# Kernel optimization log

Hardware: AMD Instinct MI355X
Metric: run time of the kernel (lower is better)

Reference implementation:

```python
import jax, jax.numpy as jnp
import numpy as np

B, H, HKV, S, D = 1, 16, 4, 2048, 128


def setup_inputs() -> dict:
    key = jax.random.key(0)
    kq, kk, kv = jax.random.split(key, 3)
    Q = jax.random.normal(kq, (B, H, S, D), dtype=jnp.float32)
    K = jax.random.normal(kk, (B, HKV, S, D), dtype=jnp.float32)
    V = jax.random.normal(kv, (B, HKV, S, D), dtype=jnp.float32)
    return {"Q": Q, "K": K, "V": V, "causal": 1, "gqa_group_size": 4}


def reference(Q, K, V, causal, gqa_group_size):
    b, h, s, d = Q.shape
    scale = 1.0 / (d ** 0.5)
    if gqa_group_size > 1:
        # repeat_interleave along head dim: [B,Hkv,S,D] -> [B,H,S,D]
        K = jnp.repeat(K, gqa_group_size, axis=1)
        V = jnp.repeat(V, gqa_group_size, axis=1)
    # scores: [B,H,S,S]
    P = jnp.einsum('bhqd,bhkd->bhqk', Q, K) * scale
    if causal:
        mask = jnp.tril(jnp.ones((s, s), dtype=bool))
        P = jnp.where(mask, P, -jnp.inf)
    P = jax.nn.softmax(P.astype(jnp.float32), axis=-1).astype(Q.dtype)
    O = jnp.einsum('bhqk,bhkd->bhqd', P, V)
    return O
```

## Files before the change

kernel.cpp:

```cpp
#include <hip/hip_runtime.h>
#include <hip/hip_bf16.h>


#define NH    16
#define NHKV  4
#define SEQ   2048
#define DIM   128
#define QBLK  64
#define KVBLK 64
#define NT    (SEQ / KVBLK)

typedef __attribute__((ext_vector_type(8))) short bf16x8_t;
typedef __attribute__((ext_vector_type(4))) float f32x4_t;

__device__ inline ushort f2bf(float f) {
    uint x = __float_as_uint(f);
    uint r = (x + 0x7fffu + ((x >> 16) & 1u)) >> 16;
    return (ushort)r;
}

#define GLOAD_LDS16(gsrc, ldst) \
    __builtin_amdgcn_global_load_lds( \
        (const __attribute__((address_space(1))) void*)(gsrc), \
        (__attribute__((address_space(3))) void*)(ldst), 16, 0, 0)

extern "C" __global__ __launch_bounds__(256)
void prep_kv(const float* __restrict__ K, const float* __restrict__ V,
             ushort* __restrict__ Kpre, ushort* __restrict__ Vpre)
{
    int gid = blockIdx.x * 256 + threadIdx.x;
    if (blockIdx.x < 1024) {
        int kvh = gid >> 16; int rem = gid & 65535;
        int s = rem >> 5; int dq = (rem & 31) << 2;
        float4 f = *(const float4*)(K + ((size_t)(kvh * SEQ + s)) * DIM + dq);
        uint lo = (uint)f2bf(f.x) | ((uint)f2bf(f.y) << 16);
        uint hi = (uint)f2bf(f.z) | ((uint)f2bf(f.w) << 16);
        int tile = s >> 6, row = s & 63;
        uint byte = ((uint)(row * 256 + dq * 2)) ^ ((uint)(row & 7) << 4);
        *(uint2*)((char*)Kpre + (((size_t)(kvh * NT + tile)) << 14) + byte) =
            make_uint2(lo, hi);
    } else {
        int g2 = gid - 1024 * 256;
        int kvh = g2 >> 16; int rem = g2 & 65535;
        int d = rem & 127; int t2 = rem >> 7;
        int tile = t2 >> 4; int kv = (t2 & 15) << 2;
        const float* b = V + ((size_t)(kvh * SEQ + tile * 64 + kv)) * DIM + d;
        uint lo = (uint)f2bf(b[0])       | ((uint)f2bf(b[DIM]) << 16);
        uint hi = (uint)f2bf(b[2 * DIM]) | ((uint)f2bf(b[3 * DIM]) << 16);
        uint byte = ((uint)(d * 128 + kv * 2)) ^ ((uint)(d & 7) << 4);
        *(uint2*)((char*)Vpre + (((size_t)(kvh * NT + tile)) << 14) + byte) =
            make_uint2(lo, hi);
    }
}

extern "C" __global__ __launch_bounds__(256)
void attn_fwd(const float* __restrict__ Q, const ushort* __restrict__ Kpre,
              const ushort* __restrict__ Vpre, float* __restrict__ O)
{
    const int bid = blockIdx.x;
    const int h   = bid & 15;
    const int p   = bid >> 4;
    const int qt  = (p < 16) ? p : 47 - p;
    const int kvh = h >> 2;
    const int q0  = qt * QBLK;
    const int tid  = threadIdx.x;
    const int w    = tid >> 6;
    const int lane = tid & 63;
    const int g    = lane >> 4;
    const int r    = lane & 15;

    __shared__ ushort Ksh[2][KVBLK * DIM];
    __shared__ ushort Vtsh[2][DIM * KVBLK];
    __shared__ ushort Psh[4 * 16 * 64];

    const float qscale = 0.08838834764831845f * 1.4426950408889634f;
    const uint swz = ((uint)(r & 7)) << 4;

    bf16x8_t qf[4];
    {
        const int qrow = q0 + w * 16 + r;
        const float* qp = Q + ((size_t)h * SEQ + qrow) * DIM + g * 8;
#pragma unroll
        for (int kb = 0; kb < 4; ++kb) {
            float4 f0 = *(const float4*)(qp + kb * 32);
            float4 f1 = *(const float4*)(qp + kb * 32 + 4);
            bf16x8_t a;
            a[0] = (short)f2bf(f0.x * qscale); a[1] = (short)f2bf(f0.y * qscale);
            a[2] = (short)f2bf(f0.z * qscale); a[3] = (short)f2bf(f0.w * qscale);
            a[4] = (short)f2bf(f1.x * qscale); a[5] = (short)f2bf(f1.y * qscale);
            a[6] = (short)f2bf(f1.z * qscale); a[7] = (short)f2bf(f1.w * qscale);
            qf[kb] = a;
        }
    }

    f32x4_t o_acc[8];
#pragma unroll
    for (int i = 0; i < 8; ++i) { f32x4_t z = {0.f, 0.f, 0.f, 0.f}; o_acc[i] = z; }
    float m_r = -1e30f, l_r = 0.f;

    const size_t kvbase = (size_t)kvh * NT;
    const int nt = qt + 1;

    auto stage = [&](int b, int t) {
        const char* kg = (const char*)Kpre + ((kvbase + t) << 14) + tid * 16;
        const char* vg = (const char*)Vpre + ((kvbase + t) << 14) + tid * 16;
        char* kl = (char*)&Ksh[b][0] + tid * 16;
        char* vl = (char*)&Vtsh[b][0] + tid * 16;
#pragma unroll
        for (int c = 0; c < 4; ++c) {
            GLOAD_LDS16(kg + c * 4096, kl + c * 4096);
            GLOAD_LDS16(vg + c * 4096, vl + c * 4096);
        }
    };

    char* pbase = (char*)Psh + w * 2048;

    stage(0, 0);
    __syncthreads();
    int buf = 0;

    for (int t = 0; t < nt; ++t) {
        if (t + 1 < nt) stage(buf ^ 1, t + 1);

        const bool diag = (t == nt - 1);

        f32x4_t sacc[4];
#pragma unroll
        for (int m = 0; m < 4; ++m) { f32x4_t z = {0.f, 0.f, 0.f, 0.f}; sacc[m] = z; }
        __builtin_amdgcn_s_setprio(1);
#pragma unroll
        for (int m = 0; m < 4; ++m) {
            if (diag && m > w) {
#pragma unroll
                for (int j2 = 0; j2 < 4; ++j2) sacc[m][j2] = -1e30f;
            } else {
                const int krow = m * 16 + r;
#pragma unroll
                for (int kb = 0; kb < 4; ++kb) {
                    uint byte = ((uint)(krow * 256 + (kb * 32 + g * 8) * 2)) ^ swz;
                    bf16x8_t kf = *(bf16x8_t*)((char*)&Ksh[buf][0] + byte);
                    sacc[m] = __builtin_amdgcn_mfma_f32_16x16x32_bf16(kf, qf[kb], sacc[m], 0, 0, 0);
                }
                if (diag && m == w) {
#pragma unroll
                    for (int j2 = 0; j2 < 4; ++j2)
                        if (g * 4 + j2 > r) sacc[m][j2] = -1e30f;
                }
            }
        }
        __builtin_amdgcn_s_setprio(0);

        float pmax = sacc[0][0];
#pragma unroll
        for (int m = 0; m < 4; ++m)
#pragma unroll
            for (int j2 = 0; j2 < 4; ++j2) pmax = fmaxf(pmax, sacc[m][j2]);
        pmax = fmaxf(pmax, __shfl_xor(pmax, 16, 64));
        pmax = fmaxf(pmax, __shfl_xor(pmax, 32, 64));

        if (!__all(pmax - m_r <= 8.f)) {
            float mnew = fmaxf(m_r, pmax);
            float alpha = __builtin_exp2f(m_r - mnew);
            m_r = mnew;
            l_r *= alpha;
#pragma unroll
            for (int pr = 0; pr < 4; ++pr) {
                float ao = __shfl(alpha, g * 20 + pr, 64);
#pragma unroll
                for (int nd = 0; nd < 8; ++nd) o_acc[nd][pr] *= ao;
            }
        }

        float psum = 0.f;
        uint Wd[4][2];
#pragma unroll
        for (int m = 0; m < 4; ++m) {
            float p0 = __builtin_exp2f(sacc[m][0] - m_r);
            float p1 = __builtin_exp2f(sacc[m][1] - m_r);
            float p2 = __builtin_exp2f(sacc[m][2] - m_r);
            float p3 = __builtin_exp2f(sacc[m][3] - m_r);
            psum += (p0 + p1) + (p2 + p3);
            Wd[m][0] = (uint)f2bf(p0) | ((uint)f2bf(p1) << 16);
            Wd[m][1] = (uint)f2bf(p2) | ((uint)f2bf(p3) << 16);
        }
        psum += __shfl_xor(psum, 16, 64);
        psum += __shfl_xor(psum, 32, 64);
        l_r += psum;

#pragma unroll
        for (int m = 0; m < 4; ++m) {
            uint byte = ((uint)(r * 128 + m * 32 + g * 8)) ^ swz;
            *(uint2*)(pbase + byte) = make_uint2(Wd[m][0], Wd[m][1]);
        }
        asm volatile("s_waitcnt lgkmcnt(0)" ::: "memory");

        __builtin_amdgcn_s_setprio(1);
#pragma unroll
        for (int kb = 0; kb < 2; ++kb) {
            uint pbyte = ((uint)(r * 128 + kb * 64 + g * 16)) ^ swz;
            bf16x8_t pa = *(bf16x8_t*)(pbase + pbyte);
#pragma unroll
            for (int nd = 0; nd < 8; ++nd) {
                int d = nd * 16 + r;
                uint vbyte = ((uint)(d * 128 + (kb * 32 + g * 8) * 2)) ^ swz;
                bf16x8_t vb = *(bf16x8_t*)((char*)&Vtsh[buf][0] + vbyte);
                o_acc[nd] = __builtin_amdgcn_mfma_f32_16x16x32_bf16(pa, vb, o_acc[nd], 0, 0, 0);
            }
        }
        __builtin_amdgcn_s_setprio(0);

        __syncthreads();
        buf ^= 1;
    }

#pragma unroll
    for (int pr = 0; pr < 4; ++pr) {
        float lq = __shfl(l_r, g * 20 + pr, 64);
        float inv = 1.0f / lq;
        int qrow = q0 + w * 16 + g * 4 + pr;
        float* op = O + ((size_t)h * SEQ + qrow) * DIM;
#pragma unroll
        for (int nd = 0; nd < 8; ++nd)
            op[nd * 16 + r] = o_acc[nd][pr] * inv;
    }
}

extern "C" void kernel_launch(void* const* d_in, const int* in_sizes, int n_in,
                              void* d_out, int out_size, void* d_ws, size_t ws_size,
                              hipStream_t stream) {
    const float* Q = (const float*)d_in[0];
    const float* K = (const float*)d_in[1];
    const float* V = (const float*)d_in[2];
    float* O = (float*)d_out;
    ushort* Kpre = (ushort*)d_ws;
    ushort* Vpre = (ushort*)((char*)d_ws + (2u << 20));
    prep_kv<<<2048, 256, 0, stream>>>(K, V, Kpre, Vpre);
    attn_fwd<<<dim3(512), 256, 0, stream>>>(Q, Kpre, Vpre, O);
}
```

Before: 140.9 us.

## Switch attention to 32x32 MFMA tiles with split-KV warps and register P

Reorganizes the attention kernel so each wave computes a 32x32 score tile with 32x32x16 bf16 MFMAs. The four waves split into two query halves and two KV halves, and the two KV-half partial results are merged through LDS at the end. P is converted with v_cvt_pk_bf16 and rearranged across lanes with permlane32 swaps, which removes the LDS round trip for P. The aim is fewer MFMA and LDS instructions per tile; the cost is an extra final reduction through shared memory and a possible change in register pressure and occupancy (launch bounds now request 2 blocks).

```diff
diff --git a/kernel.cpp b/kernel.cpp
--- a/kernel.cpp
+++ b/kernel.cpp
@@ -10,13 +10,19 @@
 #define KVBLK 64
 #define NT    (SEQ / KVBLK)
 
-typedef __attribute__((ext_vector_type(8))) short bf16x8_t;
-typedef __attribute__((ext_vector_type(4))) float f32x4_t;
+typedef __attribute__((ext_vector_type(8)))  short bf16x8_t;
+typedef __attribute__((ext_vector_type(16))) float f32x16_t;
 
 __device__ inline ushort f2bf(float f) {
     uint x = __float_as_uint(f);
     uint r = (x + 0x7fffu + ((x >> 16) & 1u)) >> 16;
     return (ushort)r;
+}
+
+__device__ inline uint cvtpk_bf16(float lo, float hi) {
+    uint r;
+    asm("v_cvt_pk_bf16_f32 %0, %1, %2" : "=v"(r) : "v"(lo), "v"(hi));
+    return r;
 }
 
 #define GLOAD_LDS16(gsrc, ldst) \
@@ -53,7 +59,7 @@
     }
 }
 
-extern "C" __global__ __launch_bounds__(256)
+extern "C" __global__ __launch_bounds__(256, 2)
 void attn_fwd(const float* __restrict__ Q, const ushort* __restrict__ Kpre,
               const ushort* __restrict__ Vpre, float* __restrict__ O)
 {
@@ -65,37 +71,39 @@
     const int q0  = qt * QBLK;
     const int tid  = threadIdx.x;
     const int w    = tid >> 6;
+    const int qh   = w >> 1;
+    const int kh   = w & 1;
     const int lane = tid & 63;
-    const int g    = lane >> 4;
-    const int r    = lane & 15;
-
-    __shared__ ushort Ksh[2][KVBLK * DIM];
-    __shared__ ushort Vtsh[2][DIM * KVBLK];
-    __shared__ ushort Psh[4 * 16 * 64];
+    const int q31  = lane & 31;
+    const int hi   = lane >> 5;
+
+    __shared__ char smem[65536];
+    char* smb = &smem[0];
 
     const float qscale = 0.08838834764831845f * 1.4426950408889634f;
-    const uint swz = ((uint)(r & 7)) << 4;
-
-    bf16x8_t qf[4];
+
+    bf16x8_t qf[8];
+    const int qrow = q0 + qh * 32 + q31;
     {
-        const int qrow = q0 + w * 16 + r;
-        const float* qp = Q + ((size_t)h * SEQ + qrow) * DIM + g * 8;
-#pragma unroll
-        for (int kb = 0; kb < 4; ++kb) {
-            float4 f0 = *(const float4*)(qp + kb * 32);
-            float4 f1 = *(const float4*)(qp + kb * 32 + 4);
+        const float* qp = Q + ((size_t)h * SEQ + qrow) * DIM + hi * 8;
+#pragma unroll
+        for (int ks = 0; ks < 8; ++ks) {
+            float4 f0 = *(const float4*)(qp + ks * 16);
+            float4 f1 = *(const float4*)(qp + ks * 16 + 4);
             bf16x8_t a;
             a[0] = (short)f2bf(f0.x * qscale); a[1] = (short)f2bf(f0.y * qscale);
             a[2] = (short)f2bf(f0.z * qscale); a[3] = (short)f2bf(f0.w * qscale);
             a[4] = (short)f2bf(f1.x * qscale); a[5] = (short)f2bf(f1.y * qscale);
             a[6] = (short)f2bf(f1.z * qscale); a[7] = (short)f2bf(f1.w * qscale);
-            qf[kb] = a;
+            qf[ks] = a;
         }
     }
 
-    f32x4_t o_acc[8];
-#pragma unroll
-    for (int i = 0; i < 8; ++i) { f32x4_t z = {0.f, 0.f, 0.f, 0.f}; o_acc[i] = z; }
+    f32x16_t oacc[4];
+#pragma unroll
+    for (int m = 0; m < 4; ++m)
+#pragma unroll
+        for (int i = 0; i < 16; ++i) oacc[m][i] = 0.f;
     float m_r = -1e30f, l_r = 0.f;
 
     const size_t kvbase = (size_t)kvh * NT;
@@ -104,8 +112,8 @@
     auto stage = [&](int b, int t) {
         const char* kg = (const char*)Kpre + ((kvbase + t) << 14) + tid * 16;
         const char* vg = (const char*)Vpre + ((kvbase + t) << 14) + tid * 16;
-        char* kl = (char*)&Ksh[b][0] + tid * 16;
-        char* vl = (char*)&Vtsh[b][0] + tid * 16;
+        char* kl = smb + b * 16384 + tid * 16;
+        char* vl = smb + 32768 + b * 16384 + tid * 16;
 #pragma unroll
         for (int c = 0; c < 4; ++c) {
             GLOAD_LDS16(kg + c * 4096, kl + c * 4096);
@@ -113,115 +121,132 @@
         }
     };
 
-    char* pbase = (char*)Psh + w * 2048;
-
     stage(0, 0);
     __syncthreads();
     int buf = 0;
 
+    const int  kvrow = kh * 32 + q31;
+    const uint kswz  = ((uint)(kvrow & 7)) << 4;
+
     for (int t = 0; t < nt; ++t) {
         if (t + 1 < nt) stage(buf ^ 1, t + 1);
-
         const bool diag = (t == nt - 1);
 
-        f32x4_t sacc[4];
-#pragma unroll
-        for (int m = 0; m < 4; ++m) { f32x4_t z = {0.f, 0.f, 0.f, 0.f}; sacc[m] = z; }
-        __builtin_amdgcn_s_setprio(1);
-#pragma unroll
-        for (int m = 0; m < 4; ++m) {
-            if (diag && m > w) {
-#pragma unroll
-                for (int j2 = 0; j2 < 4; ++j2) sacc[m][j2] = -1e30f;
-            } else {
-                const int krow = m * 16 + r;
-#pragma unroll
-                for (int kb = 0; kb < 4; ++kb) {
-                    uint byte = ((uint)(krow * 256 + (kb * 32 + g * 8) * 2)) ^ swz;
-                    bf16x8_t kf = *(bf16x8_t*)((char*)&Ksh[buf][0] + byte);
-                    sacc[m] = __builtin_amdgcn_mfma_f32_16x16x32_bf16(kf, qf[kb], sacc[m], 0, 0, 0);
+        if (!(diag && w == 1)) {
+            f32x16_t sacc;
+#pragma unroll
+            for (int i = 0; i < 16; ++i) sacc[i] = 0.f;
+            const char* kb = smb + buf * 16384;
+            __builtin_amdgcn_s_setprio(1);
+#pragma unroll
+            for (int ks = 0; ks < 8; ++ks) {
+                uint byte = ((uint)(kvrow * 256 + ks * 32 + hi * 16)) ^ kswz;
+                bf16x8_t kf = *(bf16x8_t*)(kb + byte);
+                sacc = __builtin_amdgcn_mfma_f32_32x32x16_bf16(kf, qf[ks], sacc, 0, 0, 0);
+            }
+            __builtin_amdgcn_s_setprio(0);
+
+            if (diag && (w == 0 || w == 3)) {
+#pragma unroll
+                for (int reg = 0; reg < 16; ++reg) {
+                    int crow = (reg & 3) + 8 * (reg >> 2) + 4 * hi;
+                    if (crow > q31) sacc[reg] = -1e30f;
                 }
-                if (diag && m == w) {
-#pragma unroll
-                    for (int j2 = 0; j2 < 4; ++j2)
-                        if (g * 4 + j2 > r) sacc[m][j2] = -1e30f;
+            }
+
+            float pmax = sacc[0];
+#pragma unroll
+            for (int i = 1; i < 16; ++i) pmax = fmaxf(pmax, sacc[i]);
+            pmax = fmaxf(pmax, __shfl_xor(pmax, 32, 64));
+
+            if (!__all(pmax - m_r <= 8.f)) {
+                float mnew = fmaxf(m_r, pmax);
+                float alpha = __builtin_exp2f(m_r - mnew);
+                m_r = mnew;
+                l_r *= alpha;
+#pragma unroll
+                for (int m = 0; m < 4; ++m)
+#pragma unroll
+                    for (int i = 0; i < 16; ++i) oacc[m][i] *= alpha;
+            }
+
+            float pv[16];
+            float psum = 0.f;
+#pragma unroll
+            for (int i = 0; i < 16; ++i) {
+                pv[i] = __builtin_exp2f(sacc[i] - m_r);
+                psum += pv[i];
+            }
+            psum += __shfl_xor(psum, 32, 64);
+            l_r += psum;
+
+            bf16x8_t pa[2];
+#pragma unroll
+            for (int hf = 0; hf < 2; ++hf) {
+                uint a0 = cvtpk_bf16(pv[hf * 8 + 0], pv[hf * 8 + 1]);
+                uint a1 = cvtpk_bf16(pv[hf * 8 + 2], pv[hf * 8 + 3]);
+                uint b0 = cvtpk_bf16(pv[hf * 8 + 4], pv[hf * 8 + 5]);
+                uint b1 = cvtpk_bf16(pv[hf * 8 + 6], pv[hf * 8 + 7]);
+                asm volatile("v_permlane32_swap_b32 %0, %1" : "+v"(a0), "+v"(b0));
+                asm volatile("v_permlane32_swap_b32 %0, %1" : "+v"(a1), "+v"(b1));
+                uint4 tmp = make_uint4(a0, a1, b0, b1);
+                pa[hf] = *(bf16x8_t*)&tmp;
+            }
+
+            const char* vb = smb + 32768 + buf * 16384;
+            __builtin_amdgcn_s_setprio(1);
+#pragma unroll
+            for (int m = 0; m < 4; ++m) {
+                const int drow = m * 32 + q31;
+                const uint vswz = ((uint)(drow & 7)) << 4;
+#pragma unroll
+                for (int ks2 = 0; ks2 < 2; ++ks2) {
+                    uint byte = ((uint)(drow * 128 + kh * 64 + ks2 * 32 + hi * 16)) ^ vswz;
+                    bf16x8_t vf = *(bf16x8_t*)(vb + byte);
+                    oacc[m] = __builtin_amdgcn_mfma_f32_32x32x16_bf16(vf, pa[ks2], oacc[m], 0, 0, 0);
                 }
             }
+            __builtin_amdgcn_s_setprio(0);
         }
-        __builtin_amdgcn_s_setprio(0);
-
-        float pmax = sacc[0][0];
-#pragma unroll
-        for (int m = 0; m < 4; ++m)
-#pragma unroll
-            for (int j2 = 0; j2 < 4; ++j2) pmax = fmaxf(pmax, sacc[m][j2]);
-        pmax = fmaxf(pmax, __shfl_xor(pmax, 16, 64));
-        pmax = fmaxf(pmax, __shfl_xor(pmax, 32, 64));
-
-        if (!__all(pmax - m_r <= 8.f)) {
-            float mnew = fmaxf(m_r, pmax);
-            float alpha = __builtin_exp2f(m_r - mnew);
-            m_r = mnew;
-            l_r *= alpha;
-#pragma unroll
-            for (int pr = 0; pr < 4; ++pr) {
-                float ao = __shfl(alpha, g * 20 + pr, 64);
-#pragma unroll
-                for (int nd = 0; nd < 8; ++nd) o_acc[nd][pr] *= ao;
-            }
-        }
-
-        float psum = 0.f;
-        uint Wd[4][2];
-#pragma unroll
-        for (int m = 0; m < 4; ++m) {
-            float p0 = __builtin_exp2f(sacc[m][0] - m_r);
-            float p1 = __builtin_exp2f(sacc[m][1] - m_r);
-            float p2 = __builtin_exp2f(sacc[m][2] - m_r);
-            float p3 = __builtin_exp2f(sacc[m][3] - m_r);
-            psum += (p0 + p1) + (p2 + p3);
-            Wd[m][0] = (uint)f2bf(p0) | ((uint)f2bf(p1) << 16);
-            Wd[m][1] = (uint)f2bf(p2) | ((uint)f2bf(p3) << 16);
-        }
-        psum += __shfl_xor(psum, 16, 64);
-        psum += __shfl_xor(psum, 32, 64);
-        l_r += psum;
-
-#pragma unroll
-        for (int m = 0; m < 4; ++m) {
-            uint byte = ((uint)(r * 128 + m * 32 + g * 8)) ^ swz;
-            *(uint2*)(pbase + byte) = make_uint2(Wd[m][0], Wd[m][1]);
-        }
-        asm volatile("s_waitcnt lgkmcnt(0)" ::: "memory");
-
-        __builtin_amdgcn_s_setprio(1);
-#pragma unroll
-        for (int kb = 0; kb < 2; ++kb) {
-            uint pbyte = ((uint)(r * 128 + kb * 64 + g * 16)) ^ swz;
-            bf16x8_t pa = *(bf16x8_t*)(pbase + pbyte);
-#pragma unroll
-            for (int nd = 0; nd < 8; ++nd) {
-                int d = nd * 16 + r;
-                uint vbyte = ((uint)(d * 128 + (kb * 32 + g * 8) * 2)) ^ swz;
-                bf16x8_t vb = *(bf16x8_t*)((char*)&Vtsh[buf][0] + vbyte);
-                o_acc[nd] = __builtin_amdgcn_mfma_f32_16x16x32_bf16(pa, vb, o_acc[nd], 0, 0, 0);
-            }
-        }
-        __builtin_amdgcn_s_setprio(0);
 
         __syncthreads();
         buf ^= 1;
     }
 
-#pragma unroll
-    for (int pr = 0; pr < 4; ++pr) {
-        float lq = __shfl(l_r, g * 20 + pr, 64);
-        float inv = 1.0f / lq;
-        int qrow = q0 + w * 16 + g * 4 + pr;
+    float* fb  = (float*)smb;
+    float* fb2 = fb + 128;
+    if (kh == 1) {
+        if (hi == 0) { fb[qh * 64 + q31] = m_r; fb[qh * 64 + 32 + q31] = l_r; }
+#pragma unroll
+        for (int m = 0; m < 4; ++m)
+#pragma unroll
+            for (int reg = 0; reg < 16; ++reg) {
+                int d = m * 32 + (reg & 3) + 8 * (reg >> 2) + 4 * hi;
+                fb2[(qh * 128 + d) * 32 + q31] = oacc[m][reg];
+            }
+    }
+    __syncthreads();
+    if (kh == 0) {
+        float m1 = fb[qh * 64 + q31];
+        float l1 = fb[qh * 64 + 32 + q31];
+        float mN = fmaxf(m_r, m1);
+        float a0 = __builtin_exp2f(m_r - mN);
+        float a1 = __builtin_exp2f(m1 - mN);
+        float inv = 1.0f / (l_r * a0 + l1 * a1);
+        a0 *= inv; a1 *= inv;
         float* op = O + ((size_t)h * SEQ + qrow) * DIM;
 #pragma unroll
-        for (int nd = 0; nd < 8; ++nd)
-            op[nd * 16 + r] = o_acc[nd][pr] * inv;
+        for (int m = 0; m < 4; ++m)
+#pragma unroll
+            for (int rq = 0; rq < 4; ++rq) {
+                int d0 = m * 32 + 8 * rq + 4 * hi;
+                float4 v;
+                v.x = oacc[m][rq * 4 + 0] * a0 + fb2[(qh * 128 + d0 + 0) * 32 + q31] * a1;
+                v.y = oacc[m][rq * 4 + 1] * a0 + fb2[(qh * 128 + d0 + 1) * 32 + q31] * a1;
+                v.z = oacc[m][rq * 4 + 2] * a0 + fb2[(qh * 128 + d0 + 2) * 32 + q31] * a1;
+                v.w = oacc[m][rq * 4 + 3] * a0 + fb2[(qh * 128 + d0 + 3) * 32 + q31] * a1;
+                *(float4*)(op + d0) = v;
+            }
     }
 }
 
```

After: 120.9 us. -14.2%, faster.
